# Kernel optimization log

Measured on AMD Instinct MI355X. Metric: run time of the kernel, lower is better.

Reference implementation:

```python
import jax, jax.numpy as jnp
import numpy as np

N_NODES = 5000
N_EDGES = 50000
HIDDEN = 64
EDGE_DIM = 16


def setup_inputs() -> dict:
    key = jax.random.key(0)
    ks = jax.random.split(key, 8)
    d = HIDDEN
    h = jax.random.normal(ks[0], (N_NODES, d), dtype=jnp.float32)
    edge_index = jax.random.randint(ks[1], (2, N_EDGES), 0, N_NODES, dtype=jnp.int64)
    edge_features = jax.random.normal(ks[2], (N_EDGES, EDGE_DIM), dtype=jnp.float32)
    # edge-network MLP: Linear(edge_dim, d) -> ReLU -> Linear(d, d*d)
    W1 = jax.random.normal(ks[3], (EDGE_DIM, d), dtype=jnp.float32) * (1.0 / np.sqrt(EDGE_DIM))
    b1 = jnp.zeros((d,), dtype=jnp.float32)
    W2 = jax.random.normal(ks[4], (d, d * d), dtype=jnp.float32) * (1.0 / np.sqrt(d))
    b2 = jnp.zeros((d * d,), dtype=jnp.float32)
    # GRUCell params (torch layout: rows = [reset; update; new])
    W_ih = jax.random.normal(ks[5], (3 * d, d), dtype=jnp.float32) * (1.0 / np.sqrt(d))
    W_hh = jax.random.normal(ks[6], (3 * d, d), dtype=jnp.float32) * (1.0 / np.sqrt(d))
    b_ih = jnp.zeros((3 * d,), dtype=jnp.float32)
    b_hh = jnp.zeros((3 * d,), dtype=jnp.float32)
    return {"h": h, "edge_index": edge_index, "edge_features": edge_features,
            "W1": W1, "b1": b1, "W2": W2, "b2": b2,
            "W_ih": W_ih, "W_hh": W_hh, "b_ih": b_ih, "b_hh": b_hh}


def reference(h, edge_index, edge_features, W1, b1, W2, b2, W_ih, W_hh, b_ih, b_hh):
    n_nodes, d = h.shape
    src, tgt = edge_index[0], edge_index[1]
    # 1) gather sender states
    h_w = h[src]  # (E, d)
    # 2-3) edge MLP -> per-edge transformation matrices (E, d, d)
    A = jax.nn.relu(edge_features @ W1 + b1) @ W2 + b2
    A = A.reshape(-1, d, d)
    # 4) per-edge matvec messages
    msg = jnp.einsum('eij,ej->ei', A, h_w)  # (E, d)
    # 5) scatter-sum aggregation per target node
    m = jax.ops.segment_sum(msg, tgt, num_segments=n_nodes)  # (N, d)
    # 6) GRUCell(m, h) - torch semantics
    gi = m @ W_ih.T + b_ih   # (N, 3d)
    gh = h @ W_hh.T + b_hh   # (N, 3d)
    i_r, i_z, i_n = jnp.split(gi, 3, axis=-1)
    h_r, h_z, h_n = jnp.split(gh, 3, axis=-1)
    r = jax.nn.sigmoid(i_r + h_r)
    z = jax.nn.sigmoid(i_z + h_z)
    n = jnp.tanh(i_n + r * h_n)
    h_new = (1.0 - z) * n + z * h
    return h_new
```

## Files before the change

### kernel.cpp

```cpp
#include <hip/hip_runtime.h>
#include <math.h>

#define N_NODES 5000
#define N_EDGES 50000
#define NPAD 5008
#define KP 4224
#define KSPLIT 3
#define POISON_I ((int)0xAAAAAAAAu)

typedef _Float16 f16x8 __attribute__((ext_vector_type(8)));
typedef _Float16 f16x2 __attribute__((ext_vector_type(2)));
typedef float    f32x4 __attribute__((ext_vector_type(4)));

static __device__ __forceinline__ f32x4 mfma16f(f16x8 a, f16x8 b, f32x4 c) {
    return __builtin_amdgcn_mfma_f32_16x16x32_f16(a, b, c, 0, 0, 0);
}

__global__ void prep_kernel(const float* __restrict__ W2, const float* __restrict__ b2,
                            const float* __restrict__ Wih, const float* __restrict__ Whh,
                            const int* __restrict__ ei,
                            _Float16* __restrict__ Br, _Float16* __restrict__ Bg2,
                            int* __restrict__ cnt) {
    int g = blockIdx.x * 256 + threadIdx.x;
    if (g < 33792) {
        int nt = g / 8448, rem = g - nt * 8448;
        int ks = rem >> 6, lane = rem & 63;
        int lo = lane & 15, q = lane >> 4;
        int i = nt * 16 + lo, kap0 = ks * 32 + q * 8;
        f16x8 v;
#pragma unroll
        for (int p = 0; p < 8; ++p) {
            int kap = kap0 + p;
            int k2 = kap >> 7, rem2 = kap & 127;
            int j = rem2 >> 1, k = k2 * 2 + (rem2 & 1);
            float x = 0.f;
            if (k < 64) x = W2[(size_t)k * 4096 + i * 64 + j];
            else if (k == 64) x = b2[i * 64 + j];
            v[p] = (_Float16)x;
        }
        *(f16x8*)(Br + (size_t)g * 8) = v;
        return;
    }
    g -= 33792;
    if (g < 3072) {
        int ct = g >> 7, ks = (g >> 6) & 1, lane = g & 63;
        int lo = lane & 15, q = lane >> 4;
        const float* src = (ct < 12) ? Wih : Whh;
        int r = ((ct < 12) ? ct : ct - 12) * 16 + lo;
        int j0 = ks * 32 + q * 8;
        f16x8 v;
#pragma unroll
        for (int p = 0; p < 8; ++p) v[p] = (_Float16)src[r * 64 + j0 + p];
        *(f16x8*)(Bg2 + (size_t)g * 8) = v;
        return;
    }
    g -= 3072;
    if (g < N_EDGES) atomicAdd(&cnt[ei[N_EDGES + g]], 1);
}

__global__ __launch_bounds__(1024) void scan_kernel(const int* __restrict__ cnt,
                                                    int* __restrict__ off,
                                                    int* __restrict__ cur) {
    __shared__ int s[1024];
    int tid = threadIdx.x;
    int base = tid * 5;
    int loc[5]; int sum = 0;
#pragma unroll
    for (int q = 0; q < 5; ++q) {
        int v = (base + q < N_NODES) ? (cnt[base + q] - POISON_I) : 0;
        loc[q] = sum; sum += v;
    }
    s[tid] = sum; __syncthreads();
    for (int d = 1; d < 1024; d <<= 1) {
        int v = (tid >= d) ? s[tid - d] : 0;
        __syncthreads();
        s[tid] += v;
        __syncthreads();
    }
    int excl = (tid > 0) ? s[tid - 1] : 0;
#pragma unroll
    for (int q = 0; q < 5; ++q)
        if (base + q < N_NODES) { off[base + q] = excl + loc[q]; cur[base + q] = excl + loc[q]; }
    if (tid == 1023) off[N_NODES] = excl + sum;
}

__global__ void scatter_kernel(const int* __restrict__ ei, int* __restrict__ cur,
                               int* __restrict__ srcp, int* __restrict__ eidp) {
    int e = blockIdx.x * 256 + threadIdx.x;
    if (e < N_EDGES) {
        int q = atomicAdd(&cur[ei[N_EDGES + e]], 1);
        srcp[q] = ei[e];
        eidp[q] = e;
    }
}

__global__ __launch_bounds__(256) void hbuild_kernel(const int* __restrict__ toff,
                                                     const int* __restrict__ srcp,
                                                     const int* __restrict__ eidp,
                                                     const float* __restrict__ ef,
                                                     const float* __restrict__ W1,
                                                     const float* __restrict__ b1,
                                                     const float* __restrict__ h,
                                                     _Float16* __restrict__ H) {
    __shared__ _Float16 tls[16][64];
    __shared__ float hls[16][64];
    int tid = threadIdx.x, kc = tid >> 6, lane = tid & 63;
    int v = blockIdx.x;
    float acc[16];
#pragma unroll
    for (int k = 0; k < 16; ++k) acc[k] = 0.f;
    float acc64 = 0.f;
    int s0 = 0, s1 = 0;
    if (v < N_NODES) { s0 = toff[v]; s1 = toff[v + 1]; }
    float w1c[16];
#pragma unroll
    for (int k = 0; k < 16; ++k) w1c[k] = W1[k * 64 + lane];
    float b1l = b1[lane];
    for (int tb = s0; tb < s1; tb += 16) {
        int tcnt = s1 - tb; if (tcnt > 16) tcnt = 16;
        int eidx[4], sidx[4];
#pragma unroll
        for (int r = 0; r < 4; ++r) {
            int idx = kc * 4 + r;
            if (idx < tcnt) {
                eidx[r] = eidp[tb + idx];
                sidx[r] = srcp[tb + idx];
            }
        }
#pragma unroll
        for (int r = 0; r < 4; ++r) {
            int idx = kc * 4 + r;
            if (idx < tcnt) {
                hls[idx][lane] = h[(size_t)sidx[r] * 64 + lane];
                const float* efr = ef + (size_t)eidx[r] * 16;
                float tacc = b1l;
#pragma unroll
                for (int k = 0; k < 16; ++k) tacc += efr[k] * w1c[k];
                tls[idx][lane] = (_Float16)fmaxf(tacc, 0.f);
            }
        }
        __syncthreads();
        int q = 0;
        for (; q + 1 < tcnt; q += 2) {
            float hv0 = hls[q][lane];
            float hv1 = hls[q + 1][lane];
            const f16x8* t0 = (const f16x8*)&tls[q][kc * 16];
            const f16x8* t1 = (const f16x8*)&tls[q + 1][kc * 16];
            f16x8 a0 = t0[0], a1 = t0[1];
            f16x8 c0 = t1[0], c1 = t1[1];
#pragma unroll
            for (int p = 0; p < 8; ++p) {
                acc[p]     += (float)a0[p] * hv0 + (float)c0[p] * hv1;
                acc[8 + p] += (float)a1[p] * hv0 + (float)c1[p] * hv1;
            }
            acc64 += hv0 + hv1;
        }
        if (q < tcnt) {
            float hv = hls[q][lane];
            const f16x8* t0 = (const f16x8*)&tls[q][kc * 16];
            f16x8 a0 = t0[0], a1 = t0[1];
#pragma unroll
            for (int p = 0; p < 8; ++p) {
                acc[p]     += (float)a0[p] * hv;
                acc[8 + p] += (float)a1[p] * hv;
            }
            acc64 += hv;
        }
        __syncthreads();
    }
    _Float16* Hv = H + (size_t)v * KP;
#pragma unroll
    for (int p = 0; p < 8; ++p) {
        f16x2 pv = { (_Float16)acc[p * 2], (_Float16)acc[p * 2 + 1] };
        *(f16x2*)(Hv + (kc * 8 + p) * 128 + lane * 2) = pv;
    }
    if (kc == 3) {
        f16x2 pv = { (_Float16)acc64, (_Float16)0.f };
        *(f16x2*)(Hv + 32 * 128 + lane * 2) = pv;
    }
}

__global__ __launch_bounds__(256) void gemm_part(const _Float16* __restrict__ H,
                                                 const _Float16* __restrict__ Br,
                                                 float* __restrict__ gp) {
    __shared__ _Float16 As[2][16 * 136];
    int tid = threadIdx.x, w = tid >> 6, lane = tid & 63;
    int lo = lane & 15, q = lane >> 4;
    int m0 = blockIdx.x * 16;
    int ksp = blockIdx.y;
    int ar = tid >> 4, ac = (tid & 15) * 8;
    const _Float16* Ag = H + (size_t)(m0 + ar) * KP + ksp * 1408 + ac;
    f32x4 acc = {0.f, 0.f, 0.f, 0.f};
    f16x8 pf = *(const f16x8*)(Ag);
    *(f16x8*)(&As[0][ar * 136 + ac]) = pf;
    __syncthreads();
    for (int c = 0; c < 11; ++c) {
        if (c + 1 < 11) pf = *(const f16x8*)(Ag + (size_t)(c + 1) * 128);
        const _Float16* Arow = &As[c & 1][lo * 136];
        int ksg = (ksp * 11 + c) * 4;
#pragma unroll
        for (int ks = 0; ks < 4; ++ks) {
            f16x8 a = *(const f16x8*)(Arow + ks * 32 + q * 8);
            f16x8 b = *(const f16x8*)(Br + ((size_t)((w * 132 + ksg + ks) * 64 + lane)) * 8);
            acc = mfma16f(a, b, acc);
        }
        if (c + 1 < 11) *(f16x8*)(&As[(c + 1) & 1][ar * 136 + ac]) = pf;
        __syncthreads();
    }
    float* gpo = gp + (size_t)ksp * NPAD * 64;
    int row4 = q * 4;
#pragma unroll
    for (int g = 0; g < 4; ++g)
        gpo[(size_t)(m0 + row4 + g) * 64 + w * 16 + lo] = acc[g];
}

__global__ __launch_bounds__(256) void gru_mfma(const float* __restrict__ gp,
                                                const float* __restrict__ h,
                                                const _Float16* __restrict__ Bg2,
                                                const float* __restrict__ bih,
                                                const float* __restrict__ bhh,
                                                float* __restrict__ out) {
    __shared__ _Float16 mls[16 * 72];
    __shared__ _Float16 hls[16 * 72];
    __shared__ float gbuf[16 * 385];
    int tid = threadIdx.x, w = tid >> 6, lane = tid & 63;
    int lo = lane & 15, q = lane >> 4;
    int m0 = blockIdx.x * 16;
#pragma unroll
    for (int r = 0; r < 4; ++r) {
        int idx = r * 256 + tid, nl = idx >> 6, j = idx & 63;
        int n = m0 + nl;
        float mv = 0.f, hv = 0.f;
        if (n < N_NODES) {
            mv = gp[(size_t)n * 64 + j] + gp[(size_t)NPAD * 64 + (size_t)n * 64 + j]
               + gp[(size_t)2 * NPAD * 64 + (size_t)n * 64 + j];
            hv = h[(size_t)n * 64 + j];
        }
        mls[nl * 72 + j] = (_Float16)mv;
        hls[nl * 72 + j] = (_Float16)hv;
    }
    __syncthreads();
    f16x8 am[2], ah[2];
    am[0] = *(const f16x8*)&mls[lo * 72 + q * 8];
    am[1] = *(const f16x8*)&mls[lo * 72 + 32 + q * 8];
    ah[0] = *(const f16x8*)&hls[lo * 72 + q * 8];
    ah[1] = *(const f16x8*)&hls[lo * 72 + 32 + q * 8];
    f32x4 zero4 = {0.f, 0.f, 0.f, 0.f};
    f32x4 acc[6] = {zero4, zero4, zero4, zero4, zero4, zero4};
#pragma unroll
    for (int j = 0; j < 3; ++j) {
        int ctg = w + 4 * j;
        int cth = 12 + w + 4 * j;
#pragma unroll
        for (int ks = 0; ks < 2; ++ks) {
            f16x8 bg = *(const f16x8*)(Bg2 + ((size_t)((ctg * 2 + ks) * 64 + lane)) * 8);
            f16x8 bh = *(const f16x8*)(Bg2 + ((size_t)((cth * 2 + ks) * 64 + lane)) * 8);
            acc[j]     = mfma16f(am[ks], bg, acc[j]);
            acc[3 + j] = mfma16f(ah[ks], bh, acc[3 + j]);
        }
    }
#pragma unroll
    for (int j = 0; j < 3; ++j) {
        int colg = (w + 4 * j) * 16 + lo;
        int colh = 192 + colg;
#pragma unroll
        for (int g = 0; g < 4; ++g) {
            gbuf[(q * 4 + g) * 385 + colg] = acc[j][g];
            gbuf[(q * 4 + g) * 385 + colh] = acc[3 + j][g];
        }
    }
    __syncthreads();
    int i = lane;
#pragma unroll
    for (int u = 0; u < 4; ++u) {
        int nl = w * 4 + u, n = m0 + nl;
        if (n >= N_NODES) continue;
        const float* gb = gbuf + nl * 385;
        float ir  = gb[i]       + bih[i];
        float iz  = gb[64 + i]  + bih[64 + i];
        float inn = gb[128 + i] + bih[128 + i];
        float hr  = gb[192 + i] + bhh[i];
        float hz  = gb[256 + i] + bhh[64 + i];
        float hn  = gb[320 + i] + bhh[128 + i];
        float hval = h[(size_t)n * 64 + i];
        float r = 1.f / (1.f + expf(-(ir + hr)));
        float z = 1.f / (1.f + expf(-(iz + hz)));
        float nn = tanhf(inn + r * hn);
        out[n * 64 + i] = (1.f - z) * nn + z * hval;
    }
}

extern "C" void kernel_launch(void* const* d_in, const int* in_sizes, int n_in,
                              void* d_out, int out_size, void* d_ws, size_t ws_size,
                              hipStream_t stream) {
    const float* h   = (const float*)d_in[0];
    const int*   ei  = (const int*)d_in[1];
    const float* ef  = (const float*)d_in[2];
    const float* W1  = (const float*)d_in[3];
    const float* b1  = (const float*)d_in[4];
    const float* W2  = (const float*)d_in[5];
    const float* b2  = (const float*)d_in[6];
    const float* Wih = (const float*)d_in[7];
    const float* Whh = (const float*)d_in[8];
    const float* bih = (const float*)d_in[9];
    const float* bhh = (const float*)d_in[10];
    float* out = (float*)d_out;

    _Float16* H    = (_Float16*)d_ws;
    _Float16* Br   = H + (size_t)NPAD * KP;
    _Float16* Bg2  = Br + 270336;
    float*    gp   = (float*)(Bg2 + 24576);
    int*      cnt  = (int*)(gp + (size_t)3 * NPAD * 64);
    int*      toff = cnt + N_NODES;
    int*      cur  = toff + N_NODES + 1;
    int*      srcp = cur + N_NODES;
    int*      eidp = srcp + N_EDGES;

    prep_kernel<<<340, 256, 0, stream>>>(W2, b2, Wih, Whh, ei, Br, Bg2, cnt);
    scan_kernel<<<1, 1024, 0, stream>>>(cnt, toff, cur);
    scatter_kernel<<<196, 256, 0, stream>>>(ei, cur, srcp, eidp);
    hbuild_kernel<<<NPAD, 256, 0, stream>>>(toff, srcp, eidp, ef, W1, b1, h, H);
    gemm_part<<<dim3(313, KSPLIT), 256, 0, stream>>>(H, Br, gp);
    gru_mfma<<<313, 256, 0, stream>>>(gp, h, Bg2, bih, bhh, out);
}
```

Before: 135.3 us.

## Raise GEMM split-K to 11 and drop LDS staging for direct global loads

The node-by-K GEMM is now split into 11 K-slices of 12 MFMA steps each instead of 3, giving about 3.4k blocks instead of 939. Each wave loads its A and B fragments straight from global memory, with no shared-memory double buffering and no barriers. The GRU kernel sums all 11 partial buffers. This adds parallelism and removes sync overhead. In exchange it writes and reads more partial-sum traffic, grows the workspace, and makes the A loads uncoalesced because the four waves each re-read the same A rows.

```diff
diff --git a/kernel.cpp b/kernel.cpp
--- a/kernel.cpp
+++ b/kernel.cpp
@@ -5,7 +5,7 @@
 #define N_EDGES 50000
 #define NPAD 5008
 #define KP 4224
-#define KSPLIT 3
+#define KSPLIT 11
 #define POISON_I ((int)0xAAAAAAAAu)
 
 typedef _Float16 f16x8 __attribute__((ext_vector_type(8)));
@@ -183,31 +183,20 @@
 __global__ __launch_bounds__(256) void gemm_part(const _Float16* __restrict__ H,
                                                  const _Float16* __restrict__ Br,
                                                  float* __restrict__ gp) {
-    __shared__ _Float16 As[2][16 * 136];
     int tid = threadIdx.x, w = tid >> 6, lane = tid & 63;
     int lo = lane & 15, q = lane >> 4;
     int m0 = blockIdx.x * 16;
-    int ksp = blockIdx.y;
-    int ar = tid >> 4, ac = (tid & 15) * 8;
-    const _Float16* Ag = H + (size_t)(m0 + ar) * KP + ksp * 1408 + ac;
+    int ks0 = blockIdx.y * 12;
+    const _Float16* Ag = H + (size_t)(m0 + lo) * KP + ks0 * 32 + q * 8;
+    const _Float16* Bg = Br + ((size_t)(w * 132 + ks0) * 64 + lane) * 8;
     f32x4 acc = {0.f, 0.f, 0.f, 0.f};
-    f16x8 pf = *(const f16x8*)(Ag);
-    *(f16x8*)(&As[0][ar * 136 + ac]) = pf;
-    __syncthreads();
-    for (int c = 0; c < 11; ++c) {
-        if (c + 1 < 11) pf = *(const f16x8*)(Ag + (size_t)(c + 1) * 128);
-        const _Float16* Arow = &As[c & 1][lo * 136];
-        int ksg = (ksp * 11 + c) * 4;
-#pragma unroll
-        for (int ks = 0; ks < 4; ++ks) {
-            f16x8 a = *(const f16x8*)(Arow + ks * 32 + q * 8);
-            f16x8 b = *(const f16x8*)(Br + ((size_t)((w * 132 + ksg + ks) * 64 + lane)) * 8);
-            acc = mfma16f(a, b, acc);
-        }
-        if (c + 1 < 11) *(f16x8*)(&As[(c + 1) & 1][ar * 136 + ac]) = pf;
-        __syncthreads();
-    }
-    float* gpo = gp + (size_t)ksp * NPAD * 64;
+#pragma unroll
+    for (int s = 0; s < 12; ++s) {
+        f16x8 a = *(const f16x8*)(Ag + s * 32);
+        f16x8 b = *(const f16x8*)(Bg + (size_t)s * 512);
+        acc = mfma16f(a, b, acc);
+    }
+    float* gpo = gp + (size_t)blockIdx.y * NPAD * 64;
     int row4 = q * 4;
 #pragma unroll
     for (int g = 0; g < 4; ++g)
@@ -232,9 +221,11 @@
         int n = m0 + nl;
         float mv = 0.f, hv = 0.f;
         if (n < N_NODES) {
-            mv = gp[(size_t)n * 64 + j] + gp[(size_t)NPAD * 64 + (size_t)n * 64 + j]
-               + gp[(size_t)2 * NPAD * 64 + (size_t)n * 64 + j];
-            hv = h[(size_t)n * 64 + j];
+            size_t o = (size_t)n * 64 + j;
+#pragma unroll
+            for (int sp = 0; sp < KSPLIT; ++sp)
+                mv += gp[(size_t)sp * NPAD * 64 + o];
+            hv = h[o];
         }
         mls[nl * 72 + j] = (_Float16)mv;
         hls[nl * 72 + j] = (_Float16)hv;
@@ -310,7 +301,7 @@
     _Float16* Br   = H + (size_t)NPAD * KP;
     _Float16* Bg2  = Br + 270336;
     float*    gp   = (float*)(Bg2 + 24576);
-    int*      cnt  = (int*)(gp + (size_t)3 * NPAD * 64);
+    int*      cnt  = (int*)(gp + (size_t)KSPLIT * NPAD * 64);
     int*      toff = cnt + N_NODES;
     int*      cur  = toff + N_NODES + 1;
     int*      srcp = cur + N_NODES;
```

Result: slower. 150.5 us (+11.2%).
